# Optimization experiments

Hardware: AMD Instinct MI355X
Metric: run time of the kernel (lower is better)

Reference implementation:

```python
import jax, jax.numpy as jnp
import numpy as np

H = 4        # nhead
TEMP = 0.1   # temperature
TOP_K = 5
SHAPE_EPS = 1e-5


def _ln(x, g, b):
    m = x.mean(-1, keepdims=True)
    v = ((x - m) ** 2).mean(-1, keepdims=True)
    return (x - m) / jnp.sqrt(v + SHAPE_EPS) * g + b


def _mha(x, Wqkv, bqkv, Wo, bo):
    B, L, D = x.shape
    Dh = D // H
    qkv = x @ Wqkv.T + bqkv                     # [B,L,3D]
    q, k, v = jnp.split(qkv, 3, axis=-1)
    q = q.reshape(B, L, H, Dh)
    k = k.reshape(B, L, H, Dh)
    v = v.reshape(B, L, H, Dh)
    att = jnp.einsum('bqhd,bkhd->bhqk', q, k) * (1.0 / np.sqrt(Dh))
    att = jax.nn.softmax(att, axis=-1)
    o = jnp.einsum('bhqk,bkhd->bqhd', att, v).reshape(B, L, D)
    return o @ Wo.T + bo


def _pattern_encoder(x, cls_token, Wqkv, bqkv, Wo, bo, ln1_g, ln1_b,
                     W1, b1, W2, b2, ln2_g, ln2_b, proj_W, proj_b, proj_g, proj_bb):
    B, L, D = x.shape
    h = jnp.concatenate([jnp.broadcast_to(cls_token, (B, 1, D)), x], axis=1)  # [B,L+1,D]
    for i in range(Wqkv.shape[0]):  # num_layers=2, post-norm (PyTorch default)
        a = _mha(h, Wqkv[i], bqkv[i], Wo[i], bo[i])
        h = _ln(h + a, ln1_g[i], ln1_b[i])
        f = jax.nn.gelu(h @ W1[i].T + b1[i], approximate=False) @ W2[i].T + b2[i]
        h = _ln(h + f, ln2_g[i], ln2_b[i])
    cls_out = h[:, 0, :]
    return _ln(cls_out @ proj_W.T + proj_b, proj_g, proj_bb)  # [B,d_repr]


def _value_encoder(xm, vW1, vb1, v_g, v_b, vW2, vb2):
    hh = _ln(xm @ vW1.T + vb1, v_g, v_b)
    return jax.nn.gelu(hh, approximate=False) @ vW2.T + vb2


def setup_inputs() -> dict:
    B, L, D, DR, N, P, NL = 64, 512, 512, 128, 10000, 96, 2
    key = jax.random.key(0)
    ks = jax.random.split(key, 16)
    sc = 0.02
    inp = {
        'query': jax.random.normal(ks[0], (B, L, D), jnp.float32),
        'memory_keys': jax.random.normal(ks[1], (N, DR), jnp.float32),
        'memory_values': jax.random.normal(ks[2], (N, P, D), jnp.float32),
        'cls_token': jax.random.normal(ks[3], (1, 1, D), jnp.float32) * sc,
        'Wqkv': jax.random.normal(ks[4], (NL, 3 * D, D), jnp.float32) * sc,
        'bqkv': jnp.zeros((NL, 3 * D), jnp.float32),
        'Wo': jax.random.normal(ks[5], (NL, D, D), jnp.float32) * sc,
        'bo': jnp.zeros((NL, D), jnp.float32),
        'ln1_g': jnp.ones((NL, D), jnp.float32),
        'ln1_b': jnp.zeros((NL, D), jnp.float32),
        'W1': jax.random.normal(ks[6], (NL, 2 * D, D), jnp.float32) * sc,
        'b1': jnp.zeros((NL, 2 * D), jnp.float32),
        'W2': jax.random.normal(ks[7], (NL, D, 2 * D), jnp.float32) * sc,
        'b2': jnp.zeros((NL, D), jnp.float32),
        'ln2_g': jnp.ones((NL, D), jnp.float32),
        'ln2_b': jnp.zeros((NL, D), jnp.float32),
        'proj_W': jax.random.normal(ks[8], (DR, D), jnp.float32) * sc,
        'proj_b': jnp.zeros((DR,), jnp.float32),
        'proj_g': jnp.ones((DR,), jnp.float32),
        'proj_bb': jnp.zeros((DR,), jnp.float32),
        'vW1': jax.random.normal(ks[9], (DR, D), jnp.float32) * sc,
        'vb1': jnp.zeros((DR,), jnp.float32),
        'v_g': jnp.ones((DR,), jnp.float32),
        'v_b': jnp.zeros((DR,), jnp.float32),
        'vW2': jax.random.normal(ks[10], (DR, DR), jnp.float32) * sc,
        'vb2': jnp.zeros((DR,), jnp.float32),
        'shape_w': jnp.float32(0.5),
    }
    return inp


def reference(query, memory_keys, memory_values, cls_token, Wqkv, bqkv, Wo, bo,
              ln1_g, ln1_b, W1, b1, W2, b2, ln2_g, ln2_b,
              proj_W, proj_b, proj_g, proj_bb, vW1, vb1, v_g, v_b, vW2, vb2, shape_w):
    q_repr = _pattern_encoder(query, cls_token, Wqkv, bqkv, Wo, bo, ln1_g, ln1_b,
                              W1, b1, W2, b2, ln2_g, ln2_b, proj_W, proj_b, proj_g, proj_bb)
    q_val = _value_encoder(query.mean(axis=1), vW1, vb1, v_g, v_b, vW2, vb2)
    qk = shape_w * q_repr + (1.0 - shape_w) * q_val              # [B,DR]
    # squared euclidean distance, expanded form (same math as sum((a-b)^2))
    d = ((qk ** 2).sum(-1)[:, None]
         - 2.0 * qk @ memory_keys.T
         + (memory_keys ** 2).sum(-1)[None, :])                  # [B,N]
    sim = -d / TEMP
    top_scores, top_idx = jax.lax.top_k(sim, TOP_K)              # [B,K]
    weights = jax.nn.softmax(top_scores, axis=-1)
    retrieved = memory_values[top_idx]                           # [B,K,P,D]
    return retrieved, weights
```

## Files before the change

kernel.cpp:

```cpp
#include <hip/hip_runtime.h>
#include <math.h>

#define B_    64
#define LQ    512
#define LC    513
#define DD    512
#define HH    4
#define DH    128
#define DRr   128
#define NKEYS 10000
#define PP    96
#define TOPK  5
#define MROWS (B_*LC)
#define VTSTRIDE 544

typedef __attribute__((ext_vector_type(8))) short short8v;
typedef __attribute__((ext_vector_type(4))) float f32x4;
typedef __attribute__((ext_vector_type(16))) float f32x16;

static __device__ __forceinline__ float gelu_exact(float x) {
    return 0.5f * x * (1.0f + erff(x * 0.70710678118654752440f));
}

static __device__ __forceinline__ unsigned short f2bf(float x) {
    union { float f; unsigned u; } v; v.f = x;
    unsigned r = v.u + 0x7fff + ((v.u >> 16) & 1);
    return (unsigned short)(r >> 16);
}
static __device__ __forceinline__ float bf2f(unsigned short h) {
    union { float f; unsigned u; } v; v.u = ((unsigned)h) << 16;
    return v.f;
}
static __device__ __forceinline__ void split_bf(float x, unsigned short& hi, unsigned short& lo) {
    hi = f2bf(x);
    lo = f2bf(x - bf2f(hi));
}

static __device__ __forceinline__ void gload16(const unsigned short* g, unsigned short* l) {
    __builtin_amdgcn_global_load_lds(
        (const __attribute__((address_space(1))) unsigned*)g,
        (__attribute__((address_space(3))) unsigned*)l, 16, 0, 0);
}

__global__ __launch_bounds__(256)
void split_kernel(const float* __restrict__ x, unsigned short* __restrict__ hi,
                  unsigned short* __restrict__ lo, int n4)
{
    int i = blockIdx.x * blockDim.x + threadIdx.x;
    if (i >= n4) return;
    float4 v = ((const float4*)x)[i];
    unsigned short h0,h1,h2,h3,l0,l1,l2,l3;
    split_bf(v.x,h0,l0); split_bf(v.y,h1,l1); split_bf(v.z,h2,l2); split_bf(v.w,h3,l3);
    ((uint2*)hi)[i] = make_uint2((unsigned)h0 | ((unsigned)h1 << 16), (unsigned)h2 | ((unsigned)h3 << 16));
    ((uint2*)lo)[i] = make_uint2((unsigned)l0 | ((unsigned)l1 << 16), (unsigned)l2 | ((unsigned)l3 << 16));
}

__global__ __launch_bounds__(128)
void concat_cls(const float* __restrict__ query, const float* __restrict__ cls,
                float* __restrict__ h, unsigned short* __restrict__ h_hi,
                unsigned short* __restrict__ h_lo)
{
    int row = blockIdx.x;
    int t = threadIdx.x;
    int b = row / LC, r = row - b * LC;
    const float* src = (r == 0) ? cls : (query + ((size_t)b * LQ + (r - 1)) * DD);
    float4 v = *(const float4*)(src + t * 4);
    *(float4*)(h + (size_t)row * DD + t * 4) = v;
    unsigned short hs[4], ls[4];
    split_bf(v.x, hs[0], ls[0]); split_bf(v.y, hs[1], ls[1]);
    split_bf(v.z, hs[2], ls[2]); split_bf(v.w, hs[3], ls[3]);
    size_t o = (size_t)row * DD + t * 4;
    ((uint2*)(h_hi))[o >> 2] = make_uint2((unsigned)hs[0] | ((unsigned)hs[1]<<16),
                                          (unsigned)hs[2] | ((unsigned)hs[3]<<16));
    ((uint2*)(h_lo))[o >> 2] = make_uint2((unsigned)ls[0] | ((unsigned)ls[1]<<16),
                                          (unsigned)ls[2] | ((unsigned)ls[3]<<16));
}

#define BM 128
#define BN 128
#define BK 32

#define MFMA32(a, b, c) __builtin_amdgcn_mfma_f32_32x32x16_bf16(a, b, c, 0, 0, 0)

template<int MODE>
__global__ __launch_bounds__(256)
void gemm3(const unsigned short* __restrict__ Ahi, const unsigned short* __restrict__ Alo,
           const unsigned short* __restrict__ Whi, const unsigned short* __restrict__ Wlo,
           const float* __restrict__ bias, const float* __restrict__ res,
           float* __restrict__ Cf, unsigned short* __restrict__ Chi,
           unsigned short* __restrict__ Clo, unsigned* __restrict__ Vix,
           int M, int N, int K)
{
    __shared__ __align__(16) unsigned short LAh[4096];
    __shared__ __align__(16) unsigned short LAl[4096];
    __shared__ __align__(16) unsigned short LBh[4096];
    __shared__ __align__(16) unsigned short LBl[4096];

    const int t = threadIdx.x;
    const int lane = t & 63, w = t >> 6;
    const int wr = w >> 1, wc = w & 1;
    const int row0 = blockIdx.x * BM, col0 = blockIdx.y * BN;

    const int srow = t >> 2;
    const int sg   = t & 3;
    const int glog = sg ^ (srow & 3);
    int ar0 = row0 + srow;      if (ar0 >= M) ar0 = M - 1;
    int ar1 = row0 + srow + 64; if (ar1 >= M) ar1 = M - 1;
    const size_t aoff0 = (size_t)ar0 * K + glog * 8;
    const size_t aoff1 = (size_t)ar1 * K + glog * 8;
    const size_t boff0 = (size_t)(col0 + srow) * K + glog * 8;
    const size_t boff1 = (size_t)(col0 + srow + 64) * K + glog * 8;
    const int ldso0 = t * 8;
    const int ldso1 = t * 8 + 2048;

    f32x16 acc[2][2];
    #pragma unroll
    for (int m = 0; m < 2; m++)
        #pragma unroll
        for (int n = 0; n < 2; n++)
            #pragma unroll
            for (int i = 0; i < 16; i++) acc[m][n][i] = 0.f;

    const int cl = lane & 31;
    const int kg = lane >> 5;
    const int cl3 = cl & 3;

    const int KT = K / BK;
    for (int kt = 0; kt < KT; kt++) {
        const int k0 = kt * BK;
        __syncthreads();
        gload16(Ahi + aoff0 + k0, &LAh[ldso0]);
        gload16(Ahi + aoff1 + k0, &LAh[ldso1]);
        gload16(Alo + aoff0 + k0, &LAl[ldso0]);
        gload16(Alo + aoff1 + k0, &LAl[ldso1]);
        gload16(Whi + boff0 + k0, &LBh[ldso0]);
        gload16(Whi + boff1 + k0, &LBh[ldso1]);
        gload16(Wlo + boff0 + k0, &LBl[ldso0]);
        gload16(Wlo + boff1 + k0, &LBl[ldso1]);
        __syncthreads();

        #pragma unroll
        for (int ks = 0; ks < 2; ks++) {
            const int blkswz = ((ks * 2 + kg) ^ cl3) * 8;
            short8v ah[2], al[2], bh[2], bl[2];
            #pragma unroll
            for (int m = 0; m < 2; m++) {
                int off = (wr * 64 + m * 32 + cl) * 32 + blkswz;
                ah[m] = *(const short8v*)&LAh[off];
                al[m] = *(const short8v*)&LAl[off];
            }
            #pragma unroll
            for (int n = 0; n < 2; n++) {
                int off = (wc * 64 + n * 32 + cl) * 32 + blkswz;
                bh[n] = *(const short8v*)&LBh[off];
                bl[n] = *(const short8v*)&LBl[off];
            }
            #pragma unroll
            for (int m = 0; m < 2; m++)
                #pragma unroll
                for (int n = 0; n < 2; n++) {
                    acc[m][n] = MFMA32(ah[m], bh[n], acc[m][n]);
                    acc[m][n] = MFMA32(al[m], bh[n], acc[m][n]);
                    acc[m][n] = MFMA32(ah[m], bl[n], acc[m][n]);
                }
        }
    }

    #pragma unroll
    for (int m = 0; m < 2; m++) {
        const int rb = row0 + wr * 64 + m * 32 + 4 * kg;
        #pragma unroll
        for (int n = 0; n < 2; n++) {
            const int cc = col0 + wc * 64 + n * 32 + cl;
            const float bcol = bias[cc];
            #pragma unroll
            for (int q = 0; q < 4; q++) {
                #pragma unroll
                for (int r = 0; r < 4; r++) {
                    int row = rb + 8 * q + r;
                    if (row < M) {
                        float v = acc[m][n][q * 4 + r] + bcol;
                        if (MODE == 1) v += res[(size_t)row * N + cc];
                        if (MODE == 2) {
                            v = gelu_exact(v);
                            unsigned short hv, lv;
                            split_bf(v, hv, lv);
                            Chi[(size_t)row * N + cc] = hv;
                            Clo[(size_t)row * N + cc] = lv;
                        } else if (MODE == 3) {
                            unsigned short hv, lv;
                            split_bf(v, hv, lv);
                            if (cc < 1024) {
                                Chi[(size_t)row * 1024 + cc] = hv;
                                Clo[(size_t)row * 1024 + cc] = lv;
                            } else {
                                int da = cc - 1024, hh = da >> 7, dd = da & 127;
                                int bb = row / LC, ll = row - bb * LC;
                                size_t vi = ((size_t)((bb * HH + hh) * DH + dd)) * VTSTRIDE + ll;
                                Vix[vi] = (unsigned)hv | ((unsigned)lv << 16);
                            }
                        } else {
                            Cf[(size_t)row * N + cc] = v;
                        }
                    }
                }
            }
        }
    }
}

#define AQT 64
#define AKT 32
#define NKT2 17
#define MFMA16(a, b, c) __builtin_amdgcn_mfma_f32_16x16x32_bf16(a, b, c, 0, 0, 0)
__global__ __launch_bounds__(256)
void attn_mfma(const unsigned short* __restrict__ qkhi, const unsigned short* __restrict__ qklo,
               const unsigned* __restrict__ vtx,
               unsigned short* __restrict__ ohi, unsigned short* __restrict__ olo)
{
    __shared__ __align__(16) unsigned short SM[24064];
    #define KH(r,d) SM[(r)*136 + (d)]
    #define KL(r,d) SM[4352 + (r)*136 + (d)]
    #define VH(d,k) SM[8704 + (d)*40 + (k)]
    #define VL(d,k) SM[13824 + (d)*40 + (k)]
    #define PH(r,k) SM[18944 + (r)*40 + (k)]
    #define PL(r,k) SM[21504 + (r)*40 + (k)]
    #define OS(r,d) SM[(r)*136 + (d)]

    const int t = threadIdx.x;
    const int lane = t & 63, w = t >> 6;
    const int qt = blockIdx.x, h = blockIdx.y, b = blockIdx.z;
    const int q0 = qt * AQT;
    const int c = lane & 15, g = lane >> 4;
    const float SCALE = 0.08838834764831845f;

    short8v qh[4], ql[4];
    {
        int qrow = b * LC + q0 + w * 16 + c;
        if (qrow > MROWS - 1) qrow = MROWS - 1;
        const unsigned short* bh_ = qkhi + (size_t)qrow * 1024 + h * DH;
        const unsigned short* bl_ = qklo + (size_t)qrow * 1024 + h * DH;
        #pragma unroll
        for (int ks = 0; ks < 4; ks++) {
            qh[ks] = *(const short8v*)(bh_ + ks * 32 + g * 8);
            ql[ks] = *(const short8v*)(bl_ + ks * 32 + g * 8);
        }
    }

    float m_r[4], l_r[4];
    #pragma unroll
    for (int r = 0; r < 4; r++) { m_r[r] = -INFINITY; l_r[r] = 0.f; }
    f32x4 acc_o[8];
    #pragma unroll
    for (int n = 0; n < 8; n++) { acc_o[n][0]=0.f; acc_o[n][1]=0.f; acc_o[n][2]=0.f; acc_o[n][3]=0.f; }

    const int skr = t >> 3, skd = (t & 7) * 16;
    const int svd = t >> 1, svk = (t & 1) * 16;

    for (int kt = 0; kt < NKT2; kt++) {
        __syncthreads();
        {
            int krow = b * LC + kt * AKT + skr;
            if (krow > MROWS - 1) krow = MROWS - 1;
            const unsigned short* kb  = qkhi + (size_t)krow * 1024 + 512 + h * DH + skd;
            const unsigned short* kbl = qklo + (size_t)krow * 1024 + 512 + h * DH + skd;
            *(short8v*)&KH(skr, skd)     = *(const short8v*)kb;
            *(short8v*)&KH(skr, skd + 8) = *(const short8v*)(kb + 8);
            *(short8v*)&KL(skr, skd)     = *(const short8v*)kbl;
            *(short8v*)&KL(skr, skd + 8) = *(const short8v*)(kbl + 8);
            const unsigned* vb = vtx + ((size_t)((b * HH + h) * DH + svd)) * VTSTRIDE + kt * AKT + svk;
            uint4 a0 = *(const uint4*)(vb);
            uint4 a1 = *(const uint4*)(vb + 4);
            uint4 a2 = *(const uint4*)(vb + 8);
            uint4 a3 = *(const uint4*)(vb + 12);
            uint4 hA, hB, lA, lB;
            hA.x = (a0.x & 0xffffu) | (a0.y << 16);
            hA.y = (a0.z & 0xffffu) | (a0.w << 16);
            hA.z = (a1.x & 0xffffu) | (a1.y << 16);
            hA.w = (a1.z & 0xffffu) | (a1.w << 16);
            hB.x = (a2.x & 0xffffu) | (a2.y << 16);
            hB.y = (a2.z & 0xffffu) | (a2.w << 16);
            hB.z = (a3.x & 0xffffu) | (a3.y << 16);
            hB.w = (a3.z & 0xffffu) | (a3.w << 16);
            lA.x = (a0.x >> 16) | (a0.y & 0xffff0000u);
            lA.y = (a0.z >> 16) | (a0.w & 0xffff0000u);
            lA.z = (a1.x >> 16) | (a1.y & 0xffff0000u);
            lA.w = (a1.z >> 16) | (a1.w & 0xffff0000u);
            lB.x = (a2.x >> 16) | (a2.y & 0xffff0000u);
            lB.y = (a2.z >> 16) | (a2.w & 0xffff0000u);
            lB.z = (a3.x >> 16) | (a3.y & 0xffff0000u);
            lB.w = (a3.z >> 16) | (a3.w & 0xffff0000u);
            *(uint4*)&VH(svd, svk)     = hA;
            *(uint4*)&VH(svd, svk + 8) = hB;
            *(uint4*)&VL(svd, svk)     = lA;
            *(uint4*)&VL(svd, svk + 8) = lB;
        }
        __syncthreads();

        f32x4 s[2];
        s[0][0]=s[0][1]=s[0][2]=s[0][3]=0.f;
        s[1][0]=s[1][1]=s[1][2]=s[1][3]=0.f;
        #pragma unroll
        for (int n = 0; n < 2; n++) {
            #pragma unroll
            for (int ks = 0; ks < 4; ks++) {
                short8v kh = *(const short8v*)&KH(n * 16 + c, ks * 32 + g * 8);
                short8v kl = *(const short8v*)&KL(n * 16 + c, ks * 32 + g * 8);
                s[n] = MFMA16(qh[ks], kh, s[n]);
                s[n] = MFMA16(ql[ks], kh, s[n]);
                s[n] = MFMA16(qh[ks], kl, s[n]);
            }
        }

        #pragma unroll
        for (int n = 0; n < 2; n++) {
            bool oob = (kt * 32 + n * 16 + c) >= LC;
            #pragma unroll
            for (int r = 0; r < 4; r++) {
                float sv = s[n][r] * SCALE;
                s[n][r] = oob ? -INFINITY : sv;
            }
        }

        float alpha[4], p0v[4], p1v[4];
        #pragma unroll
        for (int r = 0; r < 4; r++) {
            float rm = fmaxf(s[0][r], s[1][r]);
            #pragma unroll
            for (int off = 1; off < 16; off <<= 1) rm = fmaxf(rm, __shfl_xor(rm, off));
            float mn = fmaxf(m_r[r], rm);
            float p0 = expf(s[0][r] - mn);
            float p1 = expf(s[1][r] - mn);
            float ts = p0 + p1;
            #pragma unroll
            for (int off = 1; off < 16; off <<= 1) ts += __shfl_xor(ts, off);
            float al = expf(m_r[r] - mn);
            m_r[r] = mn;
            l_r[r] = al * l_r[r] + ts;
            alpha[r] = al;
            p0v[r] = p0; p1v[r] = p1;
        }

        #pragma unroll
        for (int n = 0; n < 8; n++)
            #pragma unroll
            for (int r = 0; r < 4; r++) acc_o[n][r] *= alpha[r];

        #pragma unroll
        for (int r = 0; r < 4; r++) {
            unsigned short ph, pl;
            split_bf(p0v[r], ph, pl);
            PH(w * 16 + g * 4 + r, c) = ph;
            PL(w * 16 + g * 4 + r, c) = pl;
            split_bf(p1v[r], ph, pl);
            PH(w * 16 + g * 4 + r, 16 + c) = ph;
            PL(w * 16 + g * 4 + r, 16 + c) = pl;
        }
        __syncthreads();

        short8v pah = *(const short8v*)&PH(w * 16 + c, g * 8);
        short8v pal = *(const short8v*)&PL(w * 16 + c, g * 8);
        #pragma unroll
        for (int n = 0; n < 8; n++) {
            short8v vh = *(const short8v*)&VH(n * 16 + c, g * 8);
            short8v vl = *(const short8v*)&VL(n * 16 + c, g * 8);
            acc_o[n] = MFMA16(pah, vh, acc_o[n]);
            acc_o[n] = MFMA16(pal, vh, acc_o[n]);
            acc_o[n] = MFMA16(pah, vl, acc_o[n]);
        }
    }

    float inv[4];
    #pragma unroll
    for (int r = 0; r < 4; r++) inv[r] = 1.0f / l_r[r];

    const int orow = t >> 2, oc0 = (t & 3) * 32;
    #pragma unroll
    for (int pass = 0; pass < 2; pass++) {
        __syncthreads();
        #pragma unroll
        for (int n = 0; n < 8; n++)
            #pragma unroll
            for (int r = 0; r < 4; r++) {
                float v = acc_o[n][r] * inv[r];
                unsigned short hv, lv;
                split_bf(v, hv, lv);
                OS(w * 16 + g * 4 + r, n * 16 + c) = pass ? lv : hv;
            }
        __syncthreads();
        int grow = q0 + orow;
        if (grow < LC) {
            unsigned short* dst = (pass ? olo : ohi) + ((size_t)(b * LC + grow)) * DD + h * DH + oc0;
            #pragma unroll
            for (int u = 0; u < 4; u++)
                *(short8v*)(dst + u * 8) = *(const short8v*)&OS(orow, oc0 + u * 8);
        }
    }
    #undef KH
    #undef KL
    #undef VH
    #undef VL
    #undef PH
    #undef PL
    #undef OS
}

__global__ __launch_bounds__(128)
void ln512(const float* __restrict__ X, const float* __restrict__ g,
           const float* __restrict__ bb, float* __restrict__ Y,
           unsigned short* __restrict__ Yhi, unsigned short* __restrict__ Ylo)
{
    __shared__ float red[2];
    int row = blockIdx.x, t = threadIdx.x;
    const float* x = X + (size_t)row * DD;
    float4 v = *(const float4*)(x + t * 4);
    float s = v.x + v.y + v.z + v.w;
    #pragma unroll
    for (int off = 1; off < 64; off <<= 1) s += __shfl_xor(s, off);
    if ((t & 63) == 0) red[t >> 6] = s;
    __syncthreads();
    float mean = (red[0] + red[1]) * (1.0f / 512.0f);
    __syncthreads();
    float d0 = v.x - mean, d1 = v.y - mean, d2 = v.z - mean, d3 = v.w - mean;
    float s2 = d0 * d0 + d1 * d1 + d2 * d2 + d3 * d3;
    #pragma unroll
    for (int off = 1; off < 64; off <<= 1) s2 += __shfl_xor(s2, off);
    if ((t & 63) == 0) red[t >> 6] = s2;
    __syncthreads();
    float var = (red[0] + red[1]) * (1.0f / 512.0f);
    float rstd = 1.0f / sqrtf(var + 1e-5f);
    float4 gv = *(const float4*)(g + t * 4);
    float4 bv = *(const float4*)(bb + t * 4);
    float4 ov;
    ov.x = d0 * rstd * gv.x + bv.x;
    ov.y = d1 * rstd * gv.y + bv.y;
    ov.z = d2 * rstd * gv.z + bv.z;
    ov.w = d3 * rstd * gv.w + bv.w;
    size_t o = (size_t)row * DD + t * 4;
    *(float4*)(Y + o) = ov;
    unsigned short hs[4], ls[4];
    split_bf(ov.x, hs[0], ls[0]); split_bf(ov.y, hs[1], ls[1]);
    split_bf(ov.z, hs[2], ls[2]); split_bf(ov.w, hs[3], ls[3]);
    ((uint2*)Yhi)[o >> 2] = make_uint2((unsigned)hs[0] | ((unsigned)hs[1]<<16),
                                       (unsigned)hs[2] | ((unsigned)hs[3]<<16));
    ((uint2*)Ylo)[o >> 2] = make_uint2((unsigned)ls[0] | ((unsigned)ls[1]<<16),
                                       (unsigned)ls[2] | ((unsigned)ls[3]<<16));
}

__global__ __launch_bounds__(128)
void mean_part(const float* __restrict__ query, float* __restrict__ part)
{
    int b = blockIdx.x, ch = blockIdx.y, t = threadIdx.x;
    const float* base = query + ((size_t)b * LQ + ch * 64) * DD + t * 4;
    float ax = 0.f, ay = 0.f, az = 0.f, aw = 0.f;
    for (int l = 0; l < 64; l++) {
        float4 v = *(const float4*)(base + (size_t)l * DD);
        ax += v.x; ay += v.y; az += v.z; aw += v.w;
    }
    *(float4*)(part + ((size_t)(b * 8 + ch)) * DD + t * 4) = make_float4(ax, ay, az, aw);
}

__global__ __launch_bounds__(128)
void mean_fin(const float* __restrict__ part, float* __restrict__ xm)
{
    int b = blockIdx.x, t = threadIdx.x;
    float ax = 0.f, ay = 0.f, az = 0.f, aw = 0.f;
    #pragma unroll
    for (int ch = 0; ch < 8; ch++) {
        float4 v = *(const float4*)(part + ((size_t)(b * 8 + ch)) * DD + t * 4);
        ax += v.x; ay += v.y; az += v.z; aw += v.w;
    }
    *(float4*)(xm + (size_t)b * DD + t * 4) =
        make_float4(ax * (1.f/512.f), ay * (1.f/512.f), az * (1.f/512.f), aw * (1.f/512.f));
}

static __device__ __forceinline__ float block128_sum(float x, float* red, int t) {
    #pragma unroll
    for (int off = 1; off < 64; off <<= 1) x += __shfl_xor(x, off);
    if ((t & 63) == 0) red[t >> 6] = x;
    __syncthreads();
    float r = red[0] + red[1];
    __syncthreads();
    return r;
}

__global__ __launch_bounds__(128)
void proj_ln(const float* __restrict__ h, const float* __restrict__ pW, const float* __restrict__ pb,
             const float* __restrict__ pg, const float* __restrict__ pbb, float* __restrict__ q_repr)
{
    __shared__ float xs[DD];
    __shared__ float red[2];
    int b = blockIdx.x, t = threadIdx.x;
    *(float4*)&xs[t * 4] = *(const float4*)(h + (size_t)(b * LC) * DD + t * 4);
    __syncthreads();
    const float* w = pW + (size_t)t * DD;
    float acc = pb[t];
    for (int k = 0; k < DD; k += 4) {
        float4 a = *(const float4*)&xs[k];
        float4 ww = *(const float4*)(w + k);
        acc += a.x * ww.x + a.y * ww.y + a.z * ww.z + a.w * ww.w;
    }
    float mean = block128_sum(acc, red, t) * (1.f / 128.f);
    float dx = acc - mean;
    float var = block128_sum(dx * dx, red, t) * (1.f / 128.f);
    float rstd = 1.0f / sqrtf(var + 1e-5f);
    q_repr[(size_t)b * DRr + t] = dx * rstd * pg[t] + pbb[t];
}

__global__ __launch_bounds__(128)
void venc(const float* __restrict__ xm, const float* __restrict__ vW1, const float* __restrict__ vb1,
          const float* __restrict__ vg, const float* __restrict__ vb,
          const float* __restrict__ vW2, const float* __restrict__ vb2,
          float* __restrict__ q_val)
{
    __shared__ float xs[DD];
    __shared__ float hg[DRr];
    __shared__ float red[2];
    int b = blockIdx.x, t = threadIdx.x;
    *(float4*)&xs[t * 4] = *(const float4*)(xm + (size_t)b * DD + t * 4);
    __syncthreads();
    const float* w = vW1 + (size_t)t * DD;
    float acc = vb1[t];
    for (int k = 0; k < DD; k += 4) {
        float4 a = *(const float4*)&xs[k];
        float4 ww = *(const float4*)(w + k);
        acc += a.x * ww.x + a.y * ww.y + a.z * ww.z + a.w * ww.w;
    }
    float mean = block128_sum(acc, red, t) * (1.f / 128.f);
    float dx = acc - mean;
    float var = block128_sum(dx * dx, red, t) * (1.f / 128.f);
    float rstd = 1.0f / sqrtf(var + 1e-5f);
    float hn = dx * rstd * vg[t] + vb[t];
    hg[t] = gelu_exact(hn);
    __syncthreads();
    const float* w2 = vW2 + (size_t)t * DRr;
    float acc2 = vb2[t];
    for (int k = 0; k < DRr; k += 4) {
        float4 a = *(const float4*)&hg[k];
        float4 ww = *(const float4*)(w2 + k);
        acc2 += a.x * ww.x + a.y * ww.y + a.z * ww.z + a.w * ww.w;
    }
    q_val[(size_t)b * DRr + t] = acc2;
}

__global__ void combine_qk(const float* __restrict__ qr, const float* __restrict__ qv,
                           const float* __restrict__ swp, float* __restrict__ qk)
{
    int i = blockIdx.x * blockDim.x + threadIdx.x;
    if (i < B_ * DRr) {
        float sw = swp[0];
        qk[i] = sw * qr[i] + (1.f - sw) * qv[i];
    }
}

#define SIMCH 10
__global__ __launch_bounds__(256)
void sim_kernel(const float* __restrict__ qk, const float* __restrict__ mkeys, float* __restrict__ sim)
{
    __shared__ float qs[DRr];
    int b = blockIdx.x, ch = blockIdx.y, t = threadIdx.x;
    if (t < DRr) qs[t] = qk[(size_t)b * DRr + t];
    __syncthreads();
    float qn = 0.f;
    #pragma unroll 8
    for (int i = 0; i < DRr; i++) qn += qs[i] * qs[i];
    int n0 = ch * (NKEYS / SIMCH), n1 = n0 + (NKEYS / SIMCH);
    for (int n = n0 + t; n < n1; n += 256) {
        const float* kr = mkeys + (size_t)n * DRr;
        float dot = 0.f, kn = 0.f;
        #pragma unroll 8
        for (int i = 0; i < DRr; i += 4) {
            float4 kv = *(const float4*)(kr + i);
            dot += qs[i] * kv.x + qs[i + 1] * kv.y + qs[i + 2] * kv.z + qs[i + 3] * kv.w;
            kn  += kv.x * kv.x + kv.y * kv.y + kv.z * kv.z + kv.w * kv.w;
        }
        float d = qn - 2.f * dot + kn;
        sim[(size_t)b * NKEYS + n] = -d / 0.1f;
    }
}

static __device__ __forceinline__ void topk_insert(float* v, int* id, float x, int n) {
    bool better = (x > v[TOPK - 1]) || (x == v[TOPK - 1] && n < id[TOPK - 1]);
    if (better) {
        v[TOPK - 1] = x; id[TOPK - 1] = n;
        #pragma unroll
        for (int k = TOPK - 1; k > 0; k--) {
            bool sw = (v[k] > v[k - 1]) || (v[k] == v[k - 1] && id[k] < id[k - 1]);
            if (!sw) break;
            float tv = v[k]; v[k] = v[k - 1]; v[k - 1] = tv;
            int ti = id[k]; id[k] = id[k - 1]; id[k - 1] = ti;
        }
    }
}

__global__ __launch_bounds__(256)
void topk_kernel(const float* __restrict__ sim, int* __restrict__ topidx, float* __restrict__ wout)
{
    __shared__ float sv[256][TOPK];
    __shared__ int   si[256][TOPK];
    int b = blockIdx.x, t = threadIdx.x;
    float v[TOPK]; int id[TOPK];
    #pragma unroll
    for (int k = 0; k < TOPK; k++) { v[k] = -INFINITY; id[k] = 0x7fffffff; }
    for (int n = t; n < NKEYS; n += 256) {
        topk_insert(v, id, sim[(size_t)b * NKEYS + n], n);
    }
    #pragma unroll
    for (int k = 0; k < TOPK; k++) { sv[t][k] = v[k]; si[t][k] = id[k]; }
    for (int strd = 128; strd >= 1; strd >>= 1) {
        __syncthreads();
        if (t < strd) {
            #pragma unroll
            for (int k = 0; k < TOPK; k++) topk_insert(v, id, sv[t + strd][k], si[t + strd][k]);
            #pragma unroll
            for (int k = 0; k < TOPK; k++) { sv[t][k] = v[k]; si[t][k] = id[k]; }
        }
    }
    if (t == 0) {
        float m = v[0];
        float e[TOPK]; float sum = 0.f;
        #pragma unroll
        for (int k = 0; k < TOPK; k++) { e[k] = expf(v[k] - m); sum += e[k]; }
        #pragma unroll
        for (int k = 0; k < TOPK; k++) {
            wout[(size_t)b * TOPK + k] = e[k] / sum;
            topidx[b * TOPK + k] = id[k];
        }
    }
}

__global__ __launch_bounds__(128)
void gather_kernel(const float* __restrict__ mv, const int* __restrict__ topidx, float* __restrict__ out)
{
    int blk = blockIdx.x;
    int b = blk / (TOPK * PP);
    int rem = blk - b * (TOPK * PP);
    int k = rem / PP;
    int p = rem - k * PP;
    int idx = topidx[b * TOPK + k];
    const float4* src = (const float4*)(mv + ((size_t)idx * PP + p) * DD);
    float4* dst = (float4*)(out + (size_t)blk * DD);
    dst[threadIdx.x] = src[threadIdx.x];
}

extern "C" void kernel_launch(void* const* d_in, const int* in_sizes, int n_in,
                              void* d_out, int out_size, void* d_ws, size_t ws_size,
                              hipStream_t stream) {
    const float* query = (const float*)d_in[0];
    const float* mkeys = (const float*)d_in[1];
    const float* mvals = (const float*)d_in[2];
    const float* cls   = (const float*)d_in[3];
    const float* Wqkv  = (const float*)d_in[4];
    const float* bqkv  = (const float*)d_in[5];
    const float* Wo    = (const float*)d_in[6];
    const float* bo    = (const float*)d_in[7];
    const float* ln1g  = (const float*)d_in[8];
    const float* ln1b  = (const float*)d_in[9];
    const float* W1    = (const float*)d_in[10];
    const float* b1    = (const float*)d_in[11];
    const float* W2    = (const float*)d_in[12];
    const float* b2    = (const float*)d_in[13];
    const float* ln2g  = (const float*)d_in[14];
    const float* ln2b  = (const float*)d_in[15];
    const float* pW    = (const float*)d_in[16];
    const float* pb    = (const float*)d_in[17];
    const float* pg    = (const float*)d_in[18];
    const float* pbb   = (const float*)d_in[19];
    const float* vW1   = (const float*)d_in[20];
    const float* vb1   = (const float*)d_in[21];
    const float* vg    = (const float*)d_in[22];
    const float* vb    = (const float*)d_in[23];
    const float* vW2   = (const float*)d_in[24];
    const float* vb2   = (const float*)d_in[25];
    const float* swp   = (const float*)d_in[26];
    float* out = (float*)d_out;

    float* ws    = (float*)d_ws;
    float* h     = ws;
    float* preln = h + (size_t)MROWS * DD;
    unsigned short* h_hi  = (unsigned short*)(preln + (size_t)MROWS * DD);
    unsigned short* h_lo  = h_hi  + (size_t)MROWS * DD;
    unsigned short* mid_hi = h_lo + (size_t)MROWS * DD;
    unsigned short* mid_lo = mid_hi + (size_t)MROWS * 1024;
    unsigned short* qkhi  = mid_lo + (size_t)MROWS * 1024;
    unsigned short* qklo  = qkhi  + (size_t)MROWS * 1024;
    unsigned* vtx         = (unsigned*)(qklo + (size_t)MROWS * 1024);
    unsigned short* wq_hi = (unsigned short*)(vtx + (size_t)32768 * VTSTRIDE);
    unsigned short* wq_lo = wq_hi + (size_t)2 * 1536 * DD;
    unsigned short* wo_hi = wq_lo + (size_t)2 * 1536 * DD;
    unsigned short* wo_lo = wo_hi + (size_t)2 * DD * DD;
    unsigned short* w1_hi = wo_lo + (size_t)2 * DD * DD;
    unsigned short* w1_lo = w1_hi + (size_t)2 * 1024 * DD;
    unsigned short* w2_hi = w1_lo + (size_t)2 * 1024 * DD;
    unsigned short* w2_lo = w2_hi + (size_t)2 * DD * 1024;
    float* xm   = (float*)(w2_lo + (size_t)2 * DD * 1024);
    float* qval = xm   + (size_t)B_ * DD;
    float* qrep = qval + (size_t)B_ * DRr;
    float* qkc  = qrep + (size_t)B_ * DRr;
    float* simb = qkc  + (size_t)B_ * DRr;
    int*   tidx = (int*)(simb + (size_t)B_ * NKEYS);
    float* mpart = (float*)(tidx + 512);
    (void)ws_size; (void)in_sizes; (void)n_in; (void)out_size;

    {
        int n4;
        n4 = 2 * 1536 * DD / 4;
        split_kernel<<<(n4 + 255) / 256, 256, 0, stream>>>(Wqkv, wq_hi, wq_lo, n4);
        n4 = 2 * DD * DD / 4;
        split_kernel<<<(n4 + 255) / 256, 256, 0, stream>>>(Wo, wo_hi, wo_lo, n4);
        n4 = 2 * 1024 * DD / 4;
        split_kernel<<<(n4 + 255) / 256, 256, 0, stream>>>(W1, w1_hi, w1_lo, n4);
        n4 = 2 * DD * 1024 / 4;
        split_kernel<<<(n4 + 255) / 256, 256, 0, stream>>>(W2, w2_hi, w2_lo, n4);
    }

    concat_cls<<<MROWS, 128, 0, stream>>>(query, cls, h, h_hi, h_lo);

    for (int l = 0; l < 2; l++) {
        const unsigned short* wqh = wq_hi + (size_t)l * 1536 * DD;
        const unsigned short* wql = wq_lo + (size_t)l * 1536 * DD;
        const unsigned short* woh = wo_hi + (size_t)l * DD * DD;
        const unsigned short* wol = wo_lo + (size_t)l * DD * DD;
        const unsigned short* w1h = w1_hi + (size_t)l * 1024 * DD;
        const unsigned short* w1l = w1_lo + (size_t)l * 1024 * DD;
        const unsigned short* w2h = w2_hi + (size_t)l * DD * 1024;
        const unsigned short* w2l = w2_lo + (size_t)l * DD * 1024;
        const float* bq  = bqkv + (size_t)l * 1536;
        const float* bol = bo   + (size_t)l * DD;
        const float* g1  = ln1g + (size_t)l * DD;
        const float* be1 = ln1b + (size_t)l * DD;
        const float* b1l = b1   + (size_t)l * 1024;
        const float* b2l = b2   + (size_t)l * DD;
        const float* g2  = ln2g + (size_t)l * DD;
        const float* be2 = ln2b + (size_t)l * DD;

        gemm3<3><<<dim3(257, 12), 256, 0, stream>>>(h_hi, h_lo, wqh, wql, bq, nullptr,
                                                    nullptr, qkhi, qklo, vtx,
                                                    MROWS, 1536, DD);
        attn_mfma<<<dim3(9, HH, B_), 256, 0, stream>>>(qkhi, qklo, vtx, h_hi, h_lo);
        gemm3<1><<<dim3(257, 4), 256, 0, stream>>>(h_hi, h_lo, woh, wol, bol, h,
                                                   preln, nullptr, nullptr, nullptr,
                                                   MROWS, DD, DD);
        ln512<<<MROWS, 128, 0, stream>>>(preln, g1, be1, h, h_hi, h_lo);
        gemm3<2><<<dim3(257, 8), 256, 0, stream>>>(h_hi, h_lo, w1h, w1l, b1l, nullptr,
                                                   nullptr, mid_hi, mid_lo, nullptr,
                                                   MROWS, 1024, DD);
        gemm3<1><<<dim3(257, 4), 256, 0, stream>>>(mid_hi, mid_lo, w2h, w2l, b2l, h,
                                                   preln, nullptr, nullptr, nullptr,
                                                   MROWS, DD, 1024);
        ln512<<<MROWS, 128, 0, stream>>>(preln, g2, be2, h, h_hi, h_lo);
    }

    proj_ln<<<B_, 128, 0, stream>>>(h, pW, pb, pg, pbb, qrep);
    mean_part<<<dim3(B_, 8), 128, 0, stream>>>(query, mpart);
    mean_fin<<<B_, 128, 0, stream>>>(mpart, xm);
    venc<<<B_, 128, 0, stream>>>(xm, vW1, vb1, vg, vb, vW2, vb2, qval);
    combine_qk<<<(B_ * DRr + 255) / 256, 256, 0, stream>>>(qrep, qval, swp, qkc);
    sim_kernel<<<dim3(B_, SIMCH), 256, 0, stream>>>(qkc, mkeys, simb);
    topk_kernel<<<B_, 256, 0, stream>>>(simb, tidx, out + (size_t)B_ * TOPK * PP * DD);
    gather_kernel<<<B_ * TOPK * PP, 128, 0, stream>>>(mvals, tidx, out);
}
```

Measured before the change: 2.430 ms.

## Swizzle workgroups across XCDs and stage V-transpose epilogue through LDS

Linearizes the GEMM and attention grids and remaps block IDs so consecutive logical tiles land on the same XCD. The goal is better L2 reuse of shared A rows and weight tiles. In the QKV GEMM, the V-part epilogue now writes the transposed V tile into LDS first and then stores it with row-contiguous global writes. This replaces the previous strided scattered stores. The change adds extra barriers and LDS traffic in the epilogue, and the tile order in attention changes.

After: 2.415 ms. About the same (-0.6%).

```diff
diff --git a/kernel.cpp b/kernel.cpp
--- a/kernel.cpp
+++ b/kernel.cpp
@@ -34,6 +34,14 @@
 static __device__ __forceinline__ void split_bf(float x, unsigned short& hi, unsigned short& lo) {
     hi = f2bf(x);
     lo = f2bf(x - bf2f(hi));
+}
+
+static __device__ __forceinline__ int xcd_swz(int orig, int nwg) {
+    int xcd = orig & 7;
+    int lid = orig >> 3;
+    int q = nwg >> 3, r = nwg & 7;
+    int base = (xcd < r) ? xcd * (q + 1) : r * (q + 1) + (xcd - r) * q;
+    return base + lid;
 }
 
 static __device__ __forceinline__ void gload16(const unsigned short* g, unsigned short* l) {
@@ -89,17 +97,20 @@
            const float* __restrict__ bias, const float* __restrict__ res,
            float* __restrict__ Cf, unsigned short* __restrict__ Chi,
            unsigned short* __restrict__ Clo, unsigned* __restrict__ Vix,
-           int M, int N, int K)
-{
-    __shared__ __align__(16) unsigned short LAh[4096];
-    __shared__ __align__(16) unsigned short LAl[4096];
-    __shared__ __align__(16) unsigned short LBh[4096];
-    __shared__ __align__(16) unsigned short LBl[4096];
+           int M, int N, int K, int NBN)
+{
+    __shared__ __align__(16) unsigned short POOL[16384];
+    unsigned short* LAh = POOL;
+    unsigned short* LAl = POOL + 4096;
+    unsigned short* LBh = POOL + 8192;
+    unsigned short* LBl = POOL + 12288;
 
     const int t = threadIdx.x;
     const int lane = t & 63, w = t >> 6;
     const int wr = w >> 1, wc = w & 1;
-    const int row0 = blockIdx.x * BM, col0 = blockIdx.y * BN;
+    const int wg = xcd_swz(blockIdx.x, gridDim.x);
+    const int bm = wg / NBN, bn = wg - bm * NBN;
+    const int row0 = bm * BM, col0 = bn * BN;
 
     const int srow = t >> 2;
     const int sg   = t & 3;
@@ -164,6 +175,51 @@
                     acc[m][n] = MFMA32(ah[m], bl[n], acc[m][n]);
                 }
         }
+    }
+
+    if (MODE == 3 && col0 >= 1024) {
+        const int hh = (col0 - 1024) >> 7;
+        unsigned* VS = (unsigned*)POOL;
+        const int bb0 = row0 / LC;
+        const int bound = (bb0 + 1) * LC;
+        const int ddl = t >> 3, j0 = (t & 7) * 16;
+        #pragma unroll
+        for (int p = 0; p < 4; p++) {
+            __syncthreads();
+            if (wc == (p >> 1)) {
+                const int ccl = col0 + wc * 64 + (p & 1) * 32 + cl;
+                const float bcol = bias[ccl];
+                #pragma unroll
+                for (int m = 0; m < 2; m++) {
+                    const int lrb = wr * 64 + m * 32 + 4 * kg;
+                    #pragma unroll
+                    for (int q = 0; q < 4; q++)
+                        #pragma unroll
+                        for (int r = 0; r < 4; r++) {
+                            float v = ((p & 1) ? acc[m][1][q * 4 + r]
+                                               : acc[m][0][q * 4 + r]) + bcol;
+                            unsigned short hv, lv;
+                            split_bf(v, hv, lv);
+                            VS[cl * 129 + lrb + 8 * q + r] =
+                                (unsigned)hv | ((unsigned)lv << 16);
+                        }
+                }
+            }
+            __syncthreads();
+            long long vb0 = (long long)((bb0 * HH + hh) * DH + p * 32 + ddl) * VTSTRIDE
+                            - (long long)bb0 * LC;
+            long long vb1 = (long long)(((bb0 + 1) * HH + hh) * DH + p * 32 + ddl) * VTSTRIDE
+                            - (long long)(bb0 + 1) * LC;
+            #pragma unroll
+            for (int j = 0; j < 16; j++) {
+                int row = row0 + j0 + j;
+                if (row < M) {
+                    long long vi = (row < bound ? vb0 : vb1) + row;
+                    Vix[vi] = VS[ddl * 129 + j0 + j];
+                }
+            }
+        }
+        return;
     }
 
     #pragma unroll
@@ -190,15 +246,8 @@
                         } else if (MODE == 3) {
                             unsigned short hv, lv;
                             split_bf(v, hv, lv);
-                            if (cc < 1024) {
-                                Chi[(size_t)row * 1024 + cc] = hv;
-                                Clo[(size_t)row * 1024 + cc] = lv;
-                            } else {
-                                int da = cc - 1024, hh = da >> 7, dd = da & 127;
-                                int bb = row / LC, ll = row - bb * LC;
-                                size_t vi = ((size_t)((bb * HH + hh) * DH + dd)) * VTSTRIDE + ll;
-                                Vix[vi] = (unsigned)hv | ((unsigned)lv << 16);
-                            }
+                            Chi[(size_t)row * 1024 + cc] = hv;
+                            Clo[(size_t)row * 1024 + cc] = lv;
                         } else {
                             Cf[(size_t)row * N + cc] = v;
                         }
@@ -229,7 +278,10 @@
 
     const int t = threadIdx.x;
     const int lane = t & 63, w = t >> 6;
-    const int qt = blockIdx.x, h = blockIdx.y, b = blockIdx.z;
+    const int id = xcd_swz(blockIdx.x, gridDim.x);
+    const int qt = id % 9;
+    const int hb = id / 9;
+    const int h = hb & 3, b = hb >> 2;
     const int q0 = qt * AQT;
     const int c = lane & 15, g = lane >> 4;
     const float SCALE = 0.08838834764831845f;
@@ -734,20 +786,20 @@
         const float* g2  = ln2g + (size_t)l * DD;
         const float* be2 = ln2b + (size_t)l * DD;
 
-        gemm3<3><<<dim3(257, 12), 256, 0, stream>>>(h_hi, h_lo, wqh, wql, bq, nullptr,
-                                                    nullptr, qkhi, qklo, vtx,
-                                                    MROWS, 1536, DD);
-        attn_mfma<<<dim3(9, HH, B_), 256, 0, stream>>>(qkhi, qklo, vtx, h_hi, h_lo);
-        gemm3<1><<<dim3(257, 4), 256, 0, stream>>>(h_hi, h_lo, woh, wol, bol, h,
-                                                   preln, nullptr, nullptr, nullptr,
-                                                   MROWS, DD, DD);
+        gemm3<3><<<257 * 12, 256, 0, stream>>>(h_hi, h_lo, wqh, wql, bq, nullptr,
+                                               nullptr, qkhi, qklo, vtx,
+                                               MROWS, 1536, DD, 12);
+        attn_mfma<<<9 * HH * B_, 256, 0, stream>>>(qkhi, qklo, vtx, h_hi, h_lo);
+        gemm3<1><<<257 * 4, 256, 0, stream>>>(h_hi, h_lo, woh, wol, bol, h,
+                                              preln, nullptr, nullptr, nullptr,
+                                              MROWS, DD, DD, 4);
         ln512<<<MROWS, 128, 0, stream>>>(preln, g1, be1, h, h_hi, h_lo);
-        gemm3<2><<<dim3(257, 8), 256, 0, stream>>>(h_hi, h_lo, w1h, w1l, b1l, nullptr,
-                                                   nullptr, mid_hi, mid_lo, nullptr,
-                                                   MROWS, 1024, DD);
-        gemm3<1><<<dim3(257, 4), 256, 0, stream>>>(mid_hi, mid_lo, w2h, w2l, b2l, h,
-                                                   preln, nullptr, nullptr, nullptr,
-                                                   MROWS, DD, 1024);
+        gemm3<2><<<257 * 8, 256, 0, stream>>>(h_hi, h_lo, w1h, w1l, b1l, nullptr,
+                                              nullptr, mid_hi, mid_lo, nullptr,
+                                              MROWS, 1024, DD, 8);
+        gemm3<1><<<257 * 4, 256, 0, stream>>>(mid_hi, mid_lo, w2h, w2l, b2l, h,
+                                              preln, nullptr, nullptr, nullptr,
+                                              MROWS, DD, 1024, 4);
         ln512<<<MROWS, 128, 0, stream>>>(preln, g2, be2, h, h_hi, h_lo);
     }
 
```
